# Performance work log

Hardware: AMD Instinct MI355X
Metric: run time of the kernel (lower is better)

Reference implementation:

```python
import jax, jax.numpy as jnp
import numpy as np

NEG_INF = -1e9


def _gru_cell(x, h, W_ih, W_hh, b_ih, b_hh):
    # torch GRUCell math, gate order [r; z; n]
    gx = x @ W_ih.T + b_ih          # [B, 3H]
    gh = h @ W_hh.T + b_hh          # [B, 3H]
    xr, xz, xn = jnp.split(gx, 3, axis=-1)
    hr, hz, hn = jnp.split(gh, 3, axis=-1)
    r = jax.nn.sigmoid(xr + hr)
    z = jax.nn.sigmoid(xz + hz)
    n = jnp.tanh(xn + r * hn)
    return (1.0 - z) * n + z * h


def setup_inputs() -> dict:
    key = jax.random.key(0)
    ks = jax.random.split(key, 8)
    B, N, D, H, P = 64, 2048, 256, 256, 256
    s = 0.05
    return {
        "sequence": jax.random.normal(ks[0], (B, N, D), jnp.float32),
        "hidden_t": jax.random.normal(ks[1], (B, H), jnp.float32),
        "sequence_mask": jnp.ones((B, N), jnp.float32),
        "num_steps": 2,
        "W_seq": jax.random.normal(ks[2], (D, P), jnp.float32) * s,
        "W_h": jax.random.normal(ks[3], (H, P), jnp.float32) * s,
        "v_att": jax.random.normal(ks[4], (P,), jnp.float32) * s,
        "W_ih": jax.random.normal(ks[5], (3 * H, D), jnp.float32) * s,
        "W_hh": jax.random.normal(ks[6], (3 * H, H), jnp.float32) * s,
        "b_ih": jnp.zeros((3 * H,), jnp.float32),
        "b_hh": jnp.zeros((3 * H,), jnp.float32),
    }


def reference(sequence, hidden_t, sequence_mask, num_steps,
              W_seq, W_h, v_att, W_ih, W_hh, b_ih, b_hh):
    # Precompute the sequence projection once (invariant across decode steps).
    seq_proj = jnp.einsum("bnd,dp->bnp", sequence, W_seq)   # [B, N, P]
    mask_bias = jnp.where(sequence_mask > 0, 0.0, NEG_INF)  # [B, N]

    def step(h, _):
        # projection similarity: v . tanh(W1 s_i + W2 h)
        proj = jnp.tanh(seq_proj + (h @ W_h)[:, None, :])   # [B, N, P]
        scores = jnp.einsum("bnp,p->bn", proj, v_att) + mask_bias
        w = jax.nn.softmax(scores, axis=-1)                  # [B, N]
        vec = jnp.einsum("bn,bnd->bd", w, sequence)          # [B, D]
        h_new = _gru_cell(vec, h, W_ih, W_hh, b_ih, b_hh)
        return h_new, w

    _, ws = jax.lax.scan(step, hidden_t, None, length=num_steps)  # [T, B, N]
    return jnp.transpose(ws, (1, 0, 2))                            # [B, T, N]
```

## Files before the change

kernel.cpp:

```cpp
#include <hip/hip_runtime.h>
#include <cstdint>

using u16 = unsigned short;
using u32 = unsigned int;
typedef __attribute__((ext_vector_type(8))) short bf16x8;
typedef __attribute__((ext_vector_type(8))) u16 u16x8;
typedef __attribute__((ext_vector_type(16))) float f32x16;
typedef __attribute__((ext_vector_type(4))) u16 u16x4;
typedef __attribute__((ext_vector_type(4))) u32 u32x4;

#define DEV static __device__ __forceinline__

DEV u16 bf16_rne(float x) {
  u32 u = __float_as_uint(x);
  u32 r = (u + 0x7FFFu + ((u >> 16) & 1u)) >> 16;
  return (u16)r;
}
DEV float bf16f(u16 h) { return __uint_as_float(((u32)h) << 16); }

DEV u32 cvt_pk_bf16(float lo, float hi) {
  u32 d;
  asm("v_cvt_pk_bf16_f32 %0, %1, %2" : "=v"(d) : "v"(lo), "v"(hi));
  return d;
}

DEV float fast_tanh(float x) {
  float e = __expf(2.0f * x);
  return 1.0f - 2.0f / (e + 1.0f);
}
DEV float sigmoidf_(float x) { return 1.0f / (1.0f + __expf(-x)); }

__global__ __launch_bounds__(1024) void prep_seqF(const float* __restrict__ seq,
                                                  u16* __restrict__ seqF,
                                                  int N, int NCH) {
  __shared__ u16 sR[65536];
  const int b = blockIdx.y, chunk = blockIdx.x, t = threadIdx.x;
  const float* src = seq + ((long)b * N + chunk * 256) * 256;
  char* sRb = (char*)sR;
#pragma unroll
  for (int i = 0; i < 8; ++i) {
    const int idx = i * 8192 + t * 8;
    float4 x = *(const float4*)(src + idx);
    float4 y = *(const float4*)(src + idx + 4);
    u32x4 o;
    o[0] = cvt_pk_bf16(x.x, x.y);
    o[1] = cvt_pk_bf16(x.z, x.w);
    o[2] = cvt_pk_bf16(y.x, y.y);
    o[3] = cvt_pk_bf16(y.z, y.w);
    const int row = idx >> 8;
    const int colb = (idx & 255) * 2;
    *(u32x4*)(sRb + row * 512 + (colb ^ ((row & 31) << 4))) = o;
  }
  __syncthreads();
  u16* dst = seqF + ((long)(b * NCH + chunk) << 16);
#pragma unroll
  for (int i = 0; i < 8; ++i) {
    const int u = i * 1024 + t;
    const int lane = u & 63, kt = (u >> 6) & 15, t8 = u >> 10;
    const int row = t8 * 32 + (lane & 31);
    const int colb = (kt * 16 + (lane >> 5) * 8) * 2;
    u16x8 v = *(const u16x8*)(sRb + row * 512 + (colb ^ ((row & 31) << 4)));
    *(u16x8*)(dst + (long)u * 8) = v;
  }
}

__global__ __launch_bounds__(256) void prep_misc(
    const float* __restrict__ Wseq, const float* __restrict__ Wih,
    const float* __restrict__ Whh, u16* __restrict__ WfG,
    float* __restrict__ WT, float* __restrict__ UT) {
  const int bid = blockIdx.x, t = threadIdx.x;
  if (bid < 32) {
    const int unit = bid * 4 + (t >> 6);
    const int lane = t & 63, l31 = lane & 31, koct = lane >> 5;
    const int pt8 = unit >> 4, kt = unit & 15;
    u16x8 o;
#pragma unroll
    for (int e = 0; e < 8; ++e)
      o[e] = bf16_rne(
          Wseq[(long)(kt * 16 + koct * 8 + e) * 256 + pt8 * 32 + l31]);
    *(u16x8*)(WfG + (long)unit * 512 + lane * 8) = o;
  } else {
    const int g = bid - 32;
    WT[(long)t * 768 + g] = Wih[(long)g * 256 + t];
    UT[(long)t * 768 + g] = Whh[(long)g * 256 + t];
  }
}

__global__ __launch_bounds__(256) void hw_q(const float* __restrict__ h,
                                            const float* __restrict__ Wh,
                                            float* __restrict__ hw) {
  const int q = blockIdx.x, b = blockIdx.y, t = threadIdx.x;
  __shared__ float sh[256];
  __shared__ float sP[4][64];
  sh[t] = h[b * 256 + t];
  __syncthreads();
  const int j4 = t & 63, dg = t >> 6;
  const int j = q * 64 + j4;
  float g = 0.f;
#pragma unroll 4
  for (int k = dg * 64; k < dg * 64 + 64; ++k)
    g = fmaf(sh[k], Wh[(long)k * 256 + j], g);
  sP[dg][j4] = g;
  __syncthreads();
  if (t < 64)
    hw[b * 256 + q * 64 + t] = (sP[0][t] + sP[1][t]) + (sP[2][t] + sP[3][t]);
}

__global__ __launch_bounds__(1024) void bigstep(
    const u16* __restrict__ seqF, const u16* __restrict__ WfG,
    const float* __restrict__ hwbuf, const float* __restrict__ vatt,
    const float* __restrict__ mask, float* __restrict__ wbuf,
    float* __restrict__ esum, float* __restrict__ part, int N, int NCH,
    int B) {
  __shared__ u16 sW[65536];
  __shared__ float sQ[256][5];
  __shared__ float se[256], shw[256], svv[256], sredE[4];

  const int t = threadIdx.x;
  const int lane = t & 63, w = t >> 6;
  const int l31 = lane & 31, koct = lane >> 5;
  const int pg = w >> 2, ng = w & 3;
  const int b = blockIdx.y, chunk = blockIdx.x;

  u16x8 wreg[8];
#pragma unroll
  for (int i = 0; i < 8; ++i)
    wreg[i] = *(const u16x8*)(WfG + (long)(i * 1024 + t) * 8);
  if (t < 256) {
    shw[t] = hwbuf[b * 256 + t];
    svv[t] = vatt[t];
  }

  const u16* bs = seqF + ((long)(b * NCH + chunk) << 16);
  const u16* bs0 = bs + (long)ng * 16384 + lane * 8;
  const u16* bs1 = bs0 + 8192;

  u16x8 s0a, s0b, s1a, s1b, s2a, s2b, s3a, s3b;
  s0a = *(const u16x8*)(bs0 + 0 * 512);
  s0b = *(const u16x8*)(bs1 + 0 * 512);
  s1a = *(const u16x8*)(bs0 + 1 * 512);
  s1b = *(const u16x8*)(bs1 + 1 * 512);
  s2a = *(const u16x8*)(bs0 + 2 * 512);
  s2b = *(const u16x8*)(bs1 + 2 * 512);
  s3a = *(const u16x8*)(bs0 + 3 * 512);
  s3b = *(const u16x8*)(bs1 + 3 * 512);

#pragma unroll
  for (int i = 0; i < 8; ++i) *(u16x8*)(&sW[(i * 1024 + t) * 8]) = wreg[i];
  __syncthreads();

  f32x16 acc00 = (f32x16)0.f, acc01 = (f32x16)0.f, acc10 = (f32x16)0.f,
         acc11 = (f32x16)0.f;
  const u16* wbase0 = &sW[pg * 16384 + lane * 8];
  const u16* wbase1 = wbase0 + 8192;

#define STEPK(Sa, Sb, kk)                                                     \
  {                                                                           \
    bf16x8 af0 = *(const bf16x8*)(wbase0 + (kk) * 512);                       \
    bf16x8 af1 = *(const bf16x8*)(wbase1 + (kk) * 512);                       \
    bf16x8 bf0 = *(bf16x8*)&Sa;                                               \
    bf16x8 bf1 = *(bf16x8*)&Sb;                                               \
    acc00 = __builtin_amdgcn_mfma_f32_32x32x16_bf16(af0, bf0, acc00, 0, 0, 0);\
    acc01 = __builtin_amdgcn_mfma_f32_32x32x16_bf16(af0, bf1, acc01, 0, 0, 0);\
    acc10 = __builtin_amdgcn_mfma_f32_32x32x16_bf16(af1, bf0, acc10, 0, 0, 0);\
    acc11 = __builtin_amdgcn_mfma_f32_32x32x16_bf16(af1, bf1, acc11, 0, 0, 0);\
  }
#define LOADK(Sa, Sb, kk)                   \
  {                                         \
    Sa = *(const u16x8*)(bs0 + (kk) * 512); \
    Sb = *(const u16x8*)(bs1 + (kk) * 512); \
  }

#pragma unroll 1
  for (int k4 = 0; k4 < 4; ++k4) {
    const int kt = k4 * 4;
    STEPK(s0a, s0b, kt + 0);
    if (k4 < 3) LOADK(s0a, s0b, kt + 4);
    STEPK(s1a, s1b, kt + 1);
    if (k4 < 3) LOADK(s1a, s1b, kt + 5);
    STEPK(s2a, s2b, kt + 2);
    if (k4 < 3) LOADK(s2a, s2b, kt + 6);
    STEPK(s3a, s3b, kt + 3);
    if (k4 < 3) LOADK(s3a, s3b, kt + 7);
  }
#undef STEPK
#undef LOADK

  float sc0 = 0.f, sc1 = 0.f;
  {
    auto accum = [&](const f32x16& A0, const f32x16& A1, int pbase) {
#pragma unroll
      for (int r = 0; r < 16; ++r) {
        const int pidx = pbase + (r & 3) + 8 * (r >> 2) + 4 * koct;
        const float pv = svv[pidx], ph = shw[pidx];
        sc0 = fmaf(pv, fast_tanh(A0[r] + ph), sc0);
        sc1 = fmaf(pv, fast_tanh(A1[r] + ph), sc1);
      }
    };
    accum(acc00, acc01, pg * 64);
    accum(acc10, acc11, pg * 64 + 32);
  }
  sc0 += __shfl_xor(sc0, 32, 64);
  sc1 += __shfl_xor(sc1, 32, 64);
  if (koct == 0) {
    sQ[ng * 64 + l31][pg] = sc0;
    sQ[ng * 64 + 32 + l31][pg] = sc1;
  }
  __syncthreads();
  if (t < 256) {
    float s = (sQ[t][0] + sQ[t][1]) + (sQ[t][2] + sQ[t][3]);
    const long n = (long)b * N + chunk * 256 + t;
    float e = (mask[n] > 0.f) ? __expf(s) : 0.f;
    se[t] = e;
    wbuf[n] = e;
    float s4 = e;
#pragma unroll
    for (int off = 1; off < 64; off <<= 1) s4 += __shfl_xor(s4, off, 64);
    if ((t & 63) == 0) sredE[t >> 6] = s4;
  }
  __syncthreads();
  if (t == 0)
    esum[b * NCH + chunk] = (sredE[0] + sredE[1]) + (sredE[2] + sredE[3]);

  const int kt = w;
  float vd0 = 0, vd1 = 0, vd2 = 0, vd3 = 0, vd4 = 0, vd5 = 0, vd6 = 0,
        vd7 = 0;
  const u16* vb = bs + ((long)kt * 64 + lane) * 8;
#pragma unroll
  for (int t8 = 0; t8 < 8; ++t8) {
    u16x8 q = *(const u16x8*)(vb + (long)t8 * 8192);
    const float wv = se[t8 * 32 + l31];
    vd0 = fmaf(wv, bf16f((u16)q[0]), vd0);
    vd1 = fmaf(wv, bf16f((u16)q[1]), vd1);
    vd2 = fmaf(wv, bf16f((u16)q[2]), vd2);
    vd3 = fmaf(wv, bf16f((u16)q[3]), vd3);
    vd4 = fmaf(wv, bf16f((u16)q[4]), vd4);
    vd5 = fmaf(wv, bf16f((u16)q[5]), vd5);
    vd6 = fmaf(wv, bf16f((u16)q[6]), vd6);
    vd7 = fmaf(wv, bf16f((u16)q[7]), vd7);
  }
#pragma unroll
  for (int off = 1; off < 32; off <<= 1) {
    vd0 += __shfl_xor(vd0, off, 64);
    vd1 += __shfl_xor(vd1, off, 64);
    vd2 += __shfl_xor(vd2, off, 64);
    vd3 += __shfl_xor(vd3, off, 64);
    vd4 += __shfl_xor(vd4, off, 64);
    vd5 += __shfl_xor(vd5, off, 64);
    vd6 += __shfl_xor(vd6, off, 64);
    vd7 += __shfl_xor(vd7, off, 64);
  }
  if (l31 == 0) {
    float4 o0 = {vd0, vd1, vd2, vd3};
    float4 o1 = {vd4, vd5, vd6, vd7};
    float* pp = part + (long)(chunk * B + b) * 256 + kt * 16 + koct * 8;
    *(float4*)pp = o0;
    *(float4*)(pp + 4) = o1;
  }
}

__global__ __launch_bounds__(256) void finalize_gru(
    const float* __restrict__ part, const float* __restrict__ esumP, int ecnt,
    const float* __restrict__ hprev, const float* __restrict__ WT,
    const float* __restrict__ UT, const float* __restrict__ bih,
    const float* __restrict__ bhh, const float* __restrict__ wbuf,
    float* __restrict__ out, float* __restrict__ hnew, int N, int T, int step,
    int NP, int B) {
  const int q = blockIdx.x, b = blockIdx.y, t = threadIdx.x;
  __shared__ float sv[256], sh[256], sP[6][4][64];
  float S = 0.f;
  for (int i = 0; i < ecnt; ++i) S += esumP[b * ecnt + i];
  const float inv = 1.f / S;
  float a = 0.f;
  for (int cc = 0; cc < NP; ++cc) a += part[((long)cc * B + b) * 256 + t];
  sv[t] = a * inv;
  sh[t] = hprev[b * 256 + t];
  __syncthreads();
  const int j4 = t & 63, dg = t >> 6;
  const int j = q * 64 + j4;
  float g0 = 0, g1 = 0, g2 = 0, g3 = 0, g4 = 0, g5 = 0;
#pragma unroll 4
  for (int d = dg * 64; d < dg * 64 + 64; ++d) {
    const float vd = sv[d], hd = sh[d];
    const float* wr_ = WT + (long)d * 768 + j;
    const float* ur_ = UT + (long)d * 768 + j;
    g0 = fmaf(vd, wr_[0], g0);
    g1 = fmaf(vd, wr_[256], g1);
    g2 = fmaf(vd, wr_[512], g2);
    g3 = fmaf(hd, ur_[0], g3);
    g4 = fmaf(hd, ur_[256], g4);
    g5 = fmaf(hd, ur_[512], g5);
  }
  sP[0][dg][j4] = g0;
  sP[1][dg][j4] = g1;
  sP[2][dg][j4] = g2;
  sP[3][dg][j4] = g3;
  sP[4][dg][j4] = g4;
  sP[5][dg][j4] = g5;
  __syncthreads();
  if (t < 64) {
    const int jj = q * 64 + t;
    float xr = bih[jj], xz = bih[256 + jj], xn = bih[512 + jj];
    float hr = bhh[jj], hz = bhh[256 + jj], hn = bhh[512 + jj];
#pragma unroll
    for (int dgg = 0; dgg < 4; ++dgg) {
      xr += sP[0][dgg][t];
      xz += sP[1][dgg][t];
      xn += sP[2][dgg][t];
      hr += sP[3][dgg][t];
      hz += sP[4][dgg][t];
      hn += sP[5][dgg][t];
    }
    float rr = sigmoidf_(xr + hr);
    float zz = sigmoidf_(xz + hz);
    float nn = fast_tanh(xn + rr * hn);
    hnew[b * 256 + jj] = (1.f - zz) * nn + zz * sh[jj];
  }
  const long ob = ((long)b * T + step) * N;
  const int nq = N >> 2;
  for (int i = 0; i * 256 < nq; ++i) {
    const int n = q * nq + i * 256 + t;
    out[ob + n] = wbuf[(long)b * N + n] * inv;
  }
}

extern "C" void kernel_launch(void* const* d_in, const int* in_sizes, int n_in,
                              void* d_out, int out_size, void* d_ws,
                              size_t ws_size, hipStream_t stream) {
  (void)n_in;
  (void)ws_size;
  const float* seq = (const float*)d_in[0];
  const float* hidden = (const float*)d_in[1];
  const float* mask = (const float*)d_in[2];
  const float* Wseq = (const float*)d_in[4];
  const float* Wh = (const float*)d_in[5];
  const float* vatt = (const float*)d_in[6];
  const float* Wih = (const float*)d_in[7];
  const float* Whh = (const float*)d_in[8];
  const float* bih = (const float*)d_in[9];
  const float* bhh = (const float*)d_in[10];
  float* out = (float*)d_out;

  const int P = in_sizes[6];
  const int H = in_sizes[5] / P;
  const int B = in_sizes[1] / H;
  const int N = in_sizes[2] / B;
  const int T = out_size / (B * N);
  const long M = (long)B * N;
  const int NCH = N / 256;

  char* p = (char*)d_ws;
  auto alloc = [&](size_t bytes) {
    char* r = p;
    p += (bytes + 255) & ~(size_t)255;
    return r;
  };
  u16* seqF = (u16*)alloc((size_t)M * 256 * 2);
  u16* WfG = (u16*)alloc((size_t)256 * 256 * 2);
  float* WT = (float*)alloc((size_t)256 * 768 * 4);
  float* UT = (float*)alloc((size_t)256 * 768 * 4);
  float* wbuf = (float*)alloc((size_t)B * N * 4);
  float* hwbuf = (float*)alloc((size_t)B * 256 * 4);
  float* hA = (float*)alloc((size_t)B * 256 * 4);
  float* hB = (float*)alloc((size_t)B * 256 * 4);
  float* part = (float*)alloc((size_t)NCH * B * 256 * 4);
  float* esum = (float*)alloc((size_t)B * NCH * 4);
  float* hbuf[2] = {hA, hB};

  prep_seqF<<<dim3(NCH, B), dim3(1024), 0, stream>>>(seq, seqF, N, NCH);
  prep_misc<<<dim3(800), dim3(256), 0, stream>>>(Wseq, Wih, Whh, WfG, WT, UT);

  for (int t = 0; t < T; ++t) {
    const float* hcur = (t == 0) ? hidden : hbuf[(t - 1) & 1];
    hw_q<<<dim3(4, B), dim3(256), 0, stream>>>(hcur, Wh, hwbuf);
    bigstep<<<dim3(NCH, B), dim3(1024), 0, stream>>>(
        seqF, WfG, hwbuf, vatt, mask, wbuf, esum, part, N, NCH, B);
    finalize_gru<<<dim3(4, B), dim3(256), 0, stream>>>(
        part, esum, NCH, hcur, WT, UT, bih, bhh, wbuf, out, hbuf[t & 1], N, T,
        t, NCH, B);
  }
}
```

Baseline: 161.7 us.

## Fuse seq bf16 conversion and h@W_h into a two-chunk-per-block attention kernel

Removes the separate prep_seqF and hw_q launches. The first decode step now converts the fp32 sequence chunk to bf16 in LDS, computes the GEMM from there, and writes the fragment-ordered bf16 copy out for later steps. Later steps stream that copy into LDS with global_load_lds. Each block now handles two consecutive chunks and computes h@W_h itself; the projection weights are read from global memory instead of being staged in LDS. This saves launches and a full pass over the sequence, at the cost of halving the grid, repeating the h@W_h work in every block, and adding more LDS/async-load synchronisation to get right.

```diff
diff --git a/kernel.cpp b/kernel.cpp
--- a/kernel.cpp
+++ b/kernel.cpp
@@ -30,44 +30,12 @@
 }
 DEV float sigmoidf_(float x) { return 1.0f / (1.0f + __expf(-x)); }
 
-__global__ __launch_bounds__(1024) void prep_seqF(const float* __restrict__ seq,
-                                                  u16* __restrict__ seqF,
-                                                  int N, int NCH) {
-  __shared__ u16 sR[65536];
-  const int b = blockIdx.y, chunk = blockIdx.x, t = threadIdx.x;
-  const float* src = seq + ((long)b * N + chunk * 256) * 256;
-  char* sRb = (char*)sR;
-#pragma unroll
-  for (int i = 0; i < 8; ++i) {
-    const int idx = i * 8192 + t * 8;
-    float4 x = *(const float4*)(src + idx);
-    float4 y = *(const float4*)(src + idx + 4);
-    u32x4 o;
-    o[0] = cvt_pk_bf16(x.x, x.y);
-    o[1] = cvt_pk_bf16(x.z, x.w);
-    o[2] = cvt_pk_bf16(y.x, y.y);
-    o[3] = cvt_pk_bf16(y.z, y.w);
-    const int row = idx >> 8;
-    const int colb = (idx & 255) * 2;
-    *(u32x4*)(sRb + row * 512 + (colb ^ ((row & 31) << 4))) = o;
-  }
-  __syncthreads();
-  u16* dst = seqF + ((long)(b * NCH + chunk) << 16);
-#pragma unroll
-  for (int i = 0; i < 8; ++i) {
-    const int u = i * 1024 + t;
-    const int lane = u & 63, kt = (u >> 6) & 15, t8 = u >> 10;
-    const int row = t8 * 32 + (lane & 31);
-    const int colb = (kt * 16 + (lane >> 5) * 8) * 2;
-    u16x8 v = *(const u16x8*)(sRb + row * 512 + (colb ^ ((row & 31) << 4)));
-    *(u16x8*)(dst + (long)u * 8) = v;
-  }
-}
-
-__global__ __launch_bounds__(256) void prep_misc(
-    const float* __restrict__ Wseq, const float* __restrict__ Wih,
-    const float* __restrict__ Whh, u16* __restrict__ WfG,
-    float* __restrict__ WT, float* __restrict__ UT) {
+__global__ __launch_bounds__(256) void prep_w(const float* __restrict__ Wseq,
+                                              const float* __restrict__ Wih,
+                                              const float* __restrict__ Whh,
+                                              u16* __restrict__ WfG,
+                                              float* __restrict__ WT,
+                                              float* __restrict__ UT) {
   const int bid = blockIdx.x, t = threadIdx.x;
   if (bid < 32) {
     const int unit = bid * 4 + (t >> 6);
@@ -80,183 +48,216 @@
           Wseq[(long)(kt * 16 + koct * 8 + e) * 256 + pt8 * 32 + l31]);
     *(u16x8*)(WfG + (long)unit * 512 + lane * 8) = o;
   } else {
-    const int g = bid - 32;
-    WT[(long)t * 768 + g] = Wih[(long)g * 256 + t];
-    UT[(long)t * 768 + g] = Whh[(long)g * 256 + t];
-  }
-}
-
-__global__ __launch_bounds__(256) void hw_q(const float* __restrict__ h,
-                                            const float* __restrict__ Wh,
-                                            float* __restrict__ hw) {
-  const int q = blockIdx.x, b = blockIdx.y, t = threadIdx.x;
-  __shared__ float sh[256];
-  __shared__ float sP[4][64];
-  sh[t] = h[b * 256 + t];
-  __syncthreads();
-  const int j4 = t & 63, dg = t >> 6;
-  const int j = q * 64 + j4;
-  float g = 0.f;
+    const int gid = bid - 32;
+    const float* src = (gid >= 12) ? Whh : Wih;
+    float* dst = (gid >= 12) ? UT : WT;
+    const int g = (gid % 12) * 64 + (t & 63);
+    const int dq = t >> 6;
 #pragma unroll 4
-  for (int k = dg * 64; k < dg * 64 + 64; ++k)
-    g = fmaf(sh[k], Wh[(long)k * 256 + j], g);
-  sP[dg][j4] = g;
-  __syncthreads();
-  if (t < 64)
-    hw[b * 256 + q * 64 + t] = (sP[0][t] + sP[1][t]) + (sP[2][t] + sP[3][t]);
-}
-
+    for (int d = dq * 64; d < dq * 64 + 64; ++d)
+      dst[(long)d * 768 + g] = src[(long)g * 256 + d];
+  }
+}
+
+template <int STEP0>
 __global__ __launch_bounds__(1024) void bigstep(
-    const u16* __restrict__ seqF, const u16* __restrict__ WfG,
-    const float* __restrict__ hwbuf, const float* __restrict__ vatt,
+    const float* __restrict__ seq, u16* __restrict__ seqF,
+    const u16* __restrict__ WfG, const float* __restrict__ hprev,
+    const float* __restrict__ Wh, const float* __restrict__ vatt,
     const float* __restrict__ mask, float* __restrict__ wbuf,
     float* __restrict__ esum, float* __restrict__ part, int N, int NCH,
     int B) {
-  __shared__ u16 sW[65536];
+  __shared__ u16 sR[65536];
   __shared__ float sQ[256][5];
   __shared__ float se[256], shw[256], svv[256], sredE[4];
-
-  const int t = threadIdx.x;
-  const int lane = t & 63, w = t >> 6;
+  __shared__ float sHW[4][256];
+
+  const int t = threadIdx.x, lane = t & 63, w = t >> 6;
   const int l31 = lane & 31, koct = lane >> 5;
   const int pg = w >> 2, ng = w & 3;
-  const int b = blockIdx.y, chunk = blockIdx.x;
-
-  u16x8 wreg[8];
-#pragma unroll
-  for (int i = 0; i < 8; ++i)
-    wreg[i] = *(const u16x8*)(WfG + (long)(i * 1024 + t) * 8);
-  if (t < 256) {
-    shw[t] = hwbuf[b * 256 + t];
-    svv[t] = vatt[t];
-  }
-
-  const u16* bs = seqF + ((long)(b * NCH + chunk) << 16);
-  const u16* bs0 = bs + (long)ng * 16384 + lane * 8;
-  const u16* bs1 = bs0 + 8192;
-
-  u16x8 s0a, s0b, s1a, s1b, s2a, s2b, s3a, s3b;
-  s0a = *(const u16x8*)(bs0 + 0 * 512);
-  s0b = *(const u16x8*)(bs1 + 0 * 512);
-  s1a = *(const u16x8*)(bs0 + 1 * 512);
-  s1b = *(const u16x8*)(bs1 + 1 * 512);
-  s2a = *(const u16x8*)(bs0 + 2 * 512);
-  s2b = *(const u16x8*)(bs1 + 2 * 512);
-  s3a = *(const u16x8*)(bs0 + 3 * 512);
-  s3b = *(const u16x8*)(bs1 + 3 * 512);
-
-#pragma unroll
-  for (int i = 0; i < 8; ++i) *(u16x8*)(&sW[(i * 1024 + t) * 8]) = wreg[i];
+  const int b = blockIdx.y, cpair = blockIdx.x;
+  char* sRb = (char*)sR;
+
+  auto fillChunk = [&](int chunk) {
+    if constexpr (STEP0) {
+      const float* src = seq + ((long)b * N + chunk * 256) * 256;
+#pragma unroll
+      for (int i = 0; i < 8; ++i) {
+        const int idx = i * 8192 + t * 8;
+        float4 x = *(const float4*)(src + idx);
+        float4 y = *(const float4*)(src + idx + 4);
+        u32x4 o;
+        o[0] = cvt_pk_bf16(x.x, x.y);
+        o[1] = cvt_pk_bf16(x.z, x.w);
+        o[2] = cvt_pk_bf16(y.x, y.y);
+        o[3] = cvt_pk_bf16(y.z, y.w);
+        const int row = idx >> 8, colb = (idx & 255) * 2;
+        *(u32x4*)(sRb + row * 512 + (colb ^ ((row & 31) << 4))) = o;
+      }
+    } else {
+      const u16* src = seqF + ((long)(b * NCH + chunk) << 16);
+#pragma unroll
+      for (int i = 0; i < 8; ++i) {
+        const u16* g = src + ((long)(i * 1024 + t)) * 8;
+        char* l = sRb + ((size_t)(i * 1024 + (t & ~63)) * 16);
+        __builtin_amdgcn_global_load_lds(
+            (const __attribute__((address_space(1))) u32*)g,
+            (__attribute__((address_space(3))) u32*)l, 16, 0, 0);
+      }
+    }
+  };
+
+  auto writeoutChunk = [&](int chunk) {
+    u16* dst = seqF + ((long)(b * NCH + chunk) << 16);
+#pragma unroll
+    for (int i = 0; i < 8; ++i) {
+      const int u = i * 1024 + t;
+      const int ln = u & 63, kt = (u >> 6) & 15, t8 = u >> 10;
+      const int row = t8 * 32 + (ln & 31);
+      const int colb = (kt * 16 + (ln >> 5) * 8) * 2;
+      u16x8 v = *(const u16x8*)(sRb + row * 512 + (colb ^ ((row & 31) << 4)));
+      *(u16x8*)(dst + (long)u * 8) = v;
+    }
+  };
+
+  auto gemmChunk = [&](f32x16& a00, f32x16& a01, f32x16& a10, f32x16& a11) {
+    const u16* wa0 = WfG + (long)(pg * 32) * 512 + lane * 8;
+    const u16* wa1 = wa0 + 16 * 512;
+    const char* p0;
+    const char* p1;
+    int sw0 = 0, sw1 = 0, cb = 0;
+    if constexpr (STEP0) {
+      const int row0 = ng * 64 + l31, row1 = row0 + 32;
+      p0 = sRb + row0 * 512;
+      p1 = sRb + row1 * 512;
+      sw0 = (row0 & 31) << 4;
+      sw1 = (row1 & 31) << 4;
+      cb = koct * 16;
+    } else {
+      p0 = sRb + (size_t)(ng * 32768) + lane * 16;
+      p1 = p0 + 16384;
+    }
+#pragma unroll 4
+    for (int kt = 0; kt < 16; ++kt) {
+      bf16x8 af0 = *(const bf16x8*)(wa0 + kt * 512);
+      bf16x8 af1 = *(const bf16x8*)(wa1 + kt * 512);
+      bf16x8 bf0, bf1;
+      if constexpr (STEP0) {
+        bf0 = *(const bf16x8*)(p0 + ((kt * 32 + cb) ^ sw0));
+        bf1 = *(const bf16x8*)(p1 + ((kt * 32 + cb) ^ sw1));
+      } else {
+        bf0 = *(const bf16x8*)(p0 + kt * 1024);
+        bf1 = *(const bf16x8*)(p1 + kt * 1024);
+      }
+      a00 = __builtin_amdgcn_mfma_f32_32x32x16_bf16(af0, bf0, a00, 0, 0, 0);
+      a01 = __builtin_amdgcn_mfma_f32_32x32x16_bf16(af0, bf1, a01, 0, 0, 0);
+      a10 = __builtin_amdgcn_mfma_f32_32x32x16_bf16(af1, bf0, a10, 0, 0, 0);
+      a11 = __builtin_amdgcn_mfma_f32_32x32x16_bf16(af1, bf1, a11, 0, 0, 0);
+    }
+  };
+
+  auto epiChunk = [&](int chunk, const f32x16& a00, const f32x16& a01,
+                      const f32x16& a10, const f32x16& a11) {
+    float sc0 = 0.f, sc1 = 0.f;
+#pragma unroll
+    for (int r = 0; r < 16; ++r) {
+      const int pidx = pg * 64 + (r & 3) + 8 * (r >> 2) + 4 * koct;
+      const float pv = svv[pidx], ph = shw[pidx];
+      sc0 = fmaf(pv, fast_tanh(a00[r] + ph), sc0);
+      sc1 = fmaf(pv, fast_tanh(a01[r] + ph), sc1);
+    }
+#pragma unroll
+    for (int r = 0; r < 16; ++r) {
+      const int pidx = pg * 64 + 32 + (r & 3) + 8 * (r >> 2) + 4 * koct;
+      const float pv = svv[pidx], ph = shw[pidx];
+      sc0 = fmaf(pv, fast_tanh(a10[r] + ph), sc0);
+      sc1 = fmaf(pv, fast_tanh(a11[r] + ph), sc1);
+    }
+    sc0 += __shfl_xor(sc0, 32, 64);
+    sc1 += __shfl_xor(sc1, 32, 64);
+    if (koct == 0) {
+      sQ[ng * 64 + l31][pg] = sc0;
+      sQ[ng * 64 + 32 + l31][pg] = sc1;
+    }
+    __syncthreads();
+    if (t < 256) {
+      float s = (sQ[t][0] + sQ[t][1]) + (sQ[t][2] + sQ[t][3]);
+      const long n = (long)b * N + chunk * 256 + t;
+      float e = (mask[n] > 0.f) ? __expf(s) : 0.f;
+      se[t] = e;
+      wbuf[n] = e;
+      float s4 = e;
+#pragma unroll
+      for (int off = 1; off < 64; off <<= 1) s4 += __shfl_xor(s4, off, 64);
+      if ((t & 63) == 0) sredE[t >> 6] = s4;
+    }
+    __syncthreads();
+    if (t == 0)
+      esum[b * NCH + chunk] = (sredE[0] + sredE[1]) + (sredE[2] + sredE[3]);
+    const u16* bs = seqF + ((long)(b * NCH + chunk) << 16);
+    const int kt = w;
+    float vd0 = 0, vd1 = 0, vd2 = 0, vd3 = 0, vd4 = 0, vd5 = 0, vd6 = 0,
+          vd7 = 0;
+    const u16* vb = bs + ((long)kt * 64 + lane) * 8;
+#pragma unroll
+    for (int t8 = 0; t8 < 8; ++t8) {
+      u16x8 q = *(const u16x8*)(vb + (long)t8 * 8192);
+      const float wv = se[t8 * 32 + l31];
+      vd0 = fmaf(wv, bf16f((u16)q[0]), vd0);
+      vd1 = fmaf(wv, bf16f((u16)q[1]), vd1);
+      vd2 = fmaf(wv, bf16f((u16)q[2]), vd2);
+      vd3 = fmaf(wv, bf16f((u16)q[3]), vd3);
+      vd4 = fmaf(wv, bf16f((u16)q[4]), vd4);
+      vd5 = fmaf(wv, bf16f((u16)q[5]), vd5);
+      vd6 = fmaf(wv, bf16f((u16)q[6]), vd6);
+      vd7 = fmaf(wv, bf16f((u16)q[7]), vd7);
+    }
+#pragma unroll
+    for (int off = 1; off < 32; off <<= 1) {
+      vd0 += __shfl_xor(vd0, off, 64);
+      vd1 += __shfl_xor(vd1, off, 64);
+      vd2 += __shfl_xor(vd2, off, 64);
+      vd3 += __shfl_xor(vd3, off, 64);
+      vd4 += __shfl_xor(vd4, off, 64);
+      vd5 += __shfl_xor(vd5, off, 64);
+      vd6 += __shfl_xor(vd6, off, 64);
+      vd7 += __shfl_xor(vd7, off, 64);
+    }
+    if (l31 == 0) {
+      float4 o0 = {vd0, vd1, vd2, vd3};
+      float4 o1 = {vd4, vd5, vd6, vd7};
+      float* pp = part + (long)(chunk * B + b) * 256 + kt * 16 + koct * 8;
+      *(float4*)pp = o0;
+      *(float4*)(pp + 4) = o1;
+    }
+  };
+
+  const int c0 = cpair * 2, c1 = c0 + 1;
+  fillChunk(c0);
+  {
+    const int p_ = t & 255, kq = t >> 8;
+    const float* hp = hprev + b * 256 + kq * 64;
+    const float* whp = Wh + (long)kq * 64 * 256 + p_;
+    float hacc = 0.f;
+#pragma unroll 8
+    for (int k = 0; k < 64; ++k) hacc = fmaf(hp[k], whp[(long)k * 256], hacc);
+    sHW[kq][p_] = hacc;
+    if (t < 256) svv[t] = vatt[t];
+  }
   __syncthreads();
-
-  f32x16 acc00 = (f32x16)0.f, acc01 = (f32x16)0.f, acc10 = (f32x16)0.f,
-         acc11 = (f32x16)0.f;
-  const u16* wbase0 = &sW[pg * 16384 + lane * 8];
-  const u16* wbase1 = wbase0 + 8192;
-
-#define STEPK(Sa, Sb, kk)                                                     \
-  {                                                                           \
-    bf16x8 af0 = *(const bf16x8*)(wbase0 + (kk) * 512);                       \
-    bf16x8 af1 = *(const bf16x8*)(wbase1 + (kk) * 512);                       \
-    bf16x8 bf0 = *(bf16x8*)&Sa;                                               \
-    bf16x8 bf1 = *(bf16x8*)&Sb;                                               \
-    acc00 = __builtin_amdgcn_mfma_f32_32x32x16_bf16(af0, bf0, acc00, 0, 0, 0);\
-    acc01 = __builtin_amdgcn_mfma_f32_32x32x16_bf16(af0, bf1, acc01, 0, 0, 0);\
-    acc10 = __builtin_amdgcn_mfma_f32_32x32x16_bf16(af1, bf0, acc10, 0, 0, 0);\
-    acc11 = __builtin_amdgcn_mfma_f32_32x32x16_bf16(af1, bf1, acc11, 0, 0, 0);\
-  }
-#define LOADK(Sa, Sb, kk)                   \
-  {                                         \
-    Sa = *(const u16x8*)(bs0 + (kk) * 512); \
-    Sb = *(const u16x8*)(bs1 + (kk) * 512); \
-  }
-
-#pragma unroll 1
-  for (int k4 = 0; k4 < 4; ++k4) {
-    const int kt = k4 * 4;
-    STEPK(s0a, s0b, kt + 0);
-    if (k4 < 3) LOADK(s0a, s0b, kt + 4);
-    STEPK(s1a, s1b, kt + 1);
-    if (k4 < 3) LOADK(s1a, s1b, kt + 5);
-    STEPK(s2a, s2b, kt + 2);
-    if (k4 < 3) LOADK(s2a, s2b, kt + 6);
-    STEPK(s3a, s3b, kt + 3);
-    if (k4 < 3) LOADK(s3a, s3b, kt + 7);
-  }
-#undef STEPK
-#undef LOADK
-
-  float sc0 = 0.f, sc1 = 0.f;
-  {
-    auto accum = [&](const f32x16& A0, const f32x16& A1, int pbase) {
-#pragma unroll
-      for (int r = 0; r < 16; ++r) {
-        const int pidx = pbase + (r & 3) + 8 * (r >> 2) + 4 * koct;
-        const float pv = svv[pidx], ph = shw[pidx];
-        sc0 = fmaf(pv, fast_tanh(A0[r] + ph), sc0);
-        sc1 = fmaf(pv, fast_tanh(A1[r] + ph), sc1);
-      }
-    };
-    accum(acc00, acc01, pg * 64);
-    accum(acc10, acc11, pg * 64 + 32);
-  }
-  sc0 += __shfl_xor(sc0, 32, 64);
-  sc1 += __shfl_xor(sc1, 32, 64);
-  if (koct == 0) {
-    sQ[ng * 64 + l31][pg] = sc0;
-    sQ[ng * 64 + 32 + l31][pg] = sc1;
-  }
+  if (t < 256) shw[t] = (sHW[0][t] + sHW[1][t]) + (sHW[2][t] + sHW[3][t]);
+  if constexpr (STEP0) writeoutChunk(c0);
+  f32x16 a00 = (f32x16)0.f, a01 = (f32x16)0.f, a10 = (f32x16)0.f,
+         a11 = (f32x16)0.f;
+  gemmChunk(a00, a01, a10, a11);
   __syncthreads();
-  if (t < 256) {
-    float s = (sQ[t][0] + sQ[t][1]) + (sQ[t][2] + sQ[t][3]);
-    const long n = (long)b * N + chunk * 256 + t;
-    float e = (mask[n] > 0.f) ? __expf(s) : 0.f;
-    se[t] = e;
-    wbuf[n] = e;
-    float s4 = e;
-#pragma unroll
-    for (int off = 1; off < 64; off <<= 1) s4 += __shfl_xor(s4, off, 64);
-    if ((t & 63) == 0) sredE[t >> 6] = s4;
-  }
-  __syncthreads();
-  if (t == 0)
-    esum[b * NCH + chunk] = (sredE[0] + sredE[1]) + (sredE[2] + sredE[3]);
-
-  const int kt = w;
-  float vd0 = 0, vd1 = 0, vd2 = 0, vd3 = 0, vd4 = 0, vd5 = 0, vd6 = 0,
-        vd7 = 0;
-  const u16* vb = bs + ((long)kt * 64 + lane) * 8;
-#pragma unroll
-  for (int t8 = 0; t8 < 8; ++t8) {
-    u16x8 q = *(const u16x8*)(vb + (long)t8 * 8192);
-    const float wv = se[t8 * 32 + l31];
-    vd0 = fmaf(wv, bf16f((u16)q[0]), vd0);
-    vd1 = fmaf(wv, bf16f((u16)q[1]), vd1);
-    vd2 = fmaf(wv, bf16f((u16)q[2]), vd2);
-    vd3 = fmaf(wv, bf16f((u16)q[3]), vd3);
-    vd4 = fmaf(wv, bf16f((u16)q[4]), vd4);
-    vd5 = fmaf(wv, bf16f((u16)q[5]), vd5);
-    vd6 = fmaf(wv, bf16f((u16)q[6]), vd6);
-    vd7 = fmaf(wv, bf16f((u16)q[7]), vd7);
-  }
-#pragma unroll
-  for (int off = 1; off < 32; off <<= 1) {
-    vd0 += __shfl_xor(vd0, off, 64);
-    vd1 += __shfl_xor(vd1, off, 64);
-    vd2 += __shfl_xor(vd2, off, 64);
-    vd3 += __shfl_xor(vd3, off, 64);
-    vd4 += __shfl_xor(vd4, off, 64);
-    vd5 += __shfl_xor(vd5, off, 64);
-    vd6 += __shfl_xor(vd6, off, 64);
-    vd7 += __shfl_xor(vd7, off, 64);
-  }
-  if (l31 == 0) {
-    float4 o0 = {vd0, vd1, vd2, vd3};
-    float4 o1 = {vd4, vd5, vd6, vd7};
-    float* pp = part + (long)(chunk * B + b) * 256 + kt * 16 + koct * 8;
-    *(float4*)pp = o0;
-    *(float4*)(pp + 4) = o1;
-  }
+  fillChunk(c1);
+  epiChunk(c0, a00, a01, a10, a11);
+  if constexpr (STEP0) writeoutChunk(c1);
+  f32x16 b00 = (f32x16)0.f, b01 = (f32x16)0.f, b10 = (f32x16)0.f,
+         b11 = (f32x16)0.f;
+  gemmChunk(b00, b01, b10, b11);
+  epiChunk(c1, b00, b01, b10, b11);
 }
 
 __global__ __launch_bounds__(256) void finalize_gru(
@@ -360,21 +361,23 @@
   float* WT = (float*)alloc((size_t)256 * 768 * 4);
   float* UT = (float*)alloc((size_t)256 * 768 * 4);
   float* wbuf = (float*)alloc((size_t)B * N * 4);
-  float* hwbuf = (float*)alloc((size_t)B * 256 * 4);
   float* hA = (float*)alloc((size_t)B * 256 * 4);
   float* hB = (float*)alloc((size_t)B * 256 * 4);
   float* part = (float*)alloc((size_t)NCH * B * 256 * 4);
   float* esum = (float*)alloc((size_t)B * NCH * 4);
   float* hbuf[2] = {hA, hB};
 
-  prep_seqF<<<dim3(NCH, B), dim3(1024), 0, stream>>>(seq, seqF, N, NCH);
-  prep_misc<<<dim3(800), dim3(256), 0, stream>>>(Wseq, Wih, Whh, WfG, WT, UT);
+  prep_w<<<dim3(56), dim3(256), 0, stream>>>(Wseq, Wih, Whh, WfG, WT, UT);
 
   for (int t = 0; t < T; ++t) {
     const float* hcur = (t == 0) ? hidden : hbuf[(t - 1) & 1];
-    hw_q<<<dim3(4, B), dim3(256), 0, stream>>>(hcur, Wh, hwbuf);
-    bigstep<<<dim3(NCH, B), dim3(1024), 0, stream>>>(
-        seqF, WfG, hwbuf, vatt, mask, wbuf, esum, part, N, NCH, B);
+    if (t == 0) {
+      bigstep<1><<<dim3(NCH / 2, B), dim3(1024), 0, stream>>>(
+          seq, seqF, WfG, hcur, Wh, vatt, mask, wbuf, esum, part, N, NCH, B);
+    } else {
+      bigstep<0><<<dim3(NCH / 2, B), dim3(1024), 0, stream>>>(
+          seq, seqF, WfG, hcur, Wh, vatt, mask, wbuf, esum, part, N, NCH, B);
+    }
     finalize_gru<<<dim3(4, B), dim3(256), 0, stream>>>(
         part, esum, NCH, hcur, WT, UT, bih, bhh, wbuf, out, hbuf[t & 1], N, T,
         t, NCH, B);
```

Measured after the change: 161.5 us. Within noise of the previous version (-0.1%).
